# Kernel tuning notes

Hardware: AMD Instinct MI355X
Metric: run time of the kernel (lower is better)

The kernel has to match this reference:

```python
import jax, jax.numpy as jnp
import numpy as np

SIGMA = 1.2
SIGMA_SQ = jnp.float32(SIGMA * SIGMA)


def setup_inputs() -> dict:
    key = jax.random.key(0)
    k1, k2, k3 = jax.random.split(key, 3)
    X = jax.random.normal(k1, (32768, 2), dtype=jnp.float32)
    pattern_layer = jax.random.normal(k2, (8192, 2), dtype=jnp.float32)
    W2 = jax.random.normal(k3, (8192,), dtype=jnp.float32)
    return {"X": X, "pattern_layer": pattern_layer, "W2": W2}


def reference(X, pattern_layer, W2):
    # Pairwise squared distances via |a|^2 + |b|^2 - 2 a.b  -> [N, P]
    x_sq = jnp.sum(X * X, axis=1, keepdims=True)              # [N, 1]
    p_sq = jnp.sum(pattern_layer * pattern_layer, axis=1)     # [P]
    cross = X @ pattern_layer.T                               # [N, P]
    Dsq = x_sq + p_sq[None, :] - 2.0 * cross                  # [N, P]
    K = jnp.exp(-Dsq / (2.0 * SIGMA_SQ))                      # RBF kernel [N, P]
    num = K @ W2                                              # [N]
    den = jnp.sum(K, axis=1)                                  # [N]
    return num / den
```

## Files before the change

### kernel.cpp

```cpp
#include <hip/hip_runtime.h>

#define N 32768
#define P 8192
#define MX 8
#define XG 4
#define PH 2
#define THREADS (XG * PH * 64)
#define XPB (XG * MX)
#define NBLK (N / XPB)
#define PAIRS (P / 2)
#define PAIRS_PER_PH (PAIRS / PH)
#define ITERS (PAIRS_PER_PH / 64)

#define RBF_F 0.50093577808645257f

typedef float v2f __attribute__((ext_vector_type(2)));

static __device__ __forceinline__ float fast_exp2(float x) {
#if __has_builtin(__builtin_amdgcn_exp2f)
    return __builtin_amdgcn_exp2f(x);
#else
    return exp2f(x);
#endif
}

__global__ void prep_kernel(const float* __restrict__ pat,
                            const float* __restrict__ w2,
                            float4* __restrict__ c) {
    int q = blockIdx.x * blockDim.x + threadIdx.x;
    if (q < P / 2) {
        float p00 = pat[4 * q + 0], p01 = pat[4 * q + 1];
        float p10 = pat[4 * q + 2], p11 = pat[4 * q + 3];
        float4 a, b;
        a.x = 2.0f * RBF_F * p00;  a.y = 2.0f * RBF_F * p10;
        a.z = 2.0f * RBF_F * p01;  a.w = 2.0f * RBF_F * p11;
        b.x = -RBF_F * (p00 * p00 + p01 * p01);
        b.y = -RBF_F * (p10 * p10 + p11 * p11);
        b.z = w2[2 * q];           b.w = w2[2 * q + 1];
        c[2 * q]     = a;
        c[2 * q + 1] = b;
    }
}

__global__ __launch_bounds__(THREADS, 4) void
rbf_kernel(const float* __restrict__ X,
           const float4* __restrict__ c,
           float* __restrict__ out) {
    const int t    = threadIdx.x;
    const int lane = t & 63;
    const int w    = __builtin_amdgcn_readfirstlane(t >> 6);
    const int xg   = w >> 1;
    const int ph   = w & 1;

    const int xb = blockIdx.x * XPB + xg * MX;
    const float2* Xp = (const float2*)X;
    v2f xs0[MX], xs1[MX];
#pragma unroll
    for (int i = 0; i < MX; ++i) {
        float2 xv = Xp[xb + i];
        xs0[i] = (v2f){xv.x, xv.x};
        xs1[i] = (v2f){xv.y, xv.y};
    }

    v2f num2[MX], den2[MX];
#pragma unroll
    for (int i = 0; i < MX; ++i) {
        num2[i] = (v2f){0.f, 0.f};
        den2[i] = (v2f){0.f, 0.f};
    }

    const float4* __restrict__ C4w =
        c + (size_t)ph * (2 * PAIRS_PER_PH) + 2 * lane;

#pragma unroll
    for (int j = 0; j < ITERS; ++j) {
        float4 a = C4w[(j << 7)];
        float4 b = C4w[(j << 7) + 1];
#pragma unroll
        for (int i = 0; i < MX; ++i) {
            v2f tt = __builtin_elementwise_fma((v2f){a.x, a.y}, xs0[i],
                                               (v2f){b.x, b.y});
            tt = __builtin_elementwise_fma((v2f){a.z, a.w}, xs1[i], tt);
            v2f k = (v2f){fast_exp2(tt.x), fast_exp2(tt.y)};
            den2[i] += k;
            num2[i] = __builtin_elementwise_fma(k, (v2f){b.z, b.w}, num2[i]);
        }
    }

    float num[MX], den[MX];
#pragma unroll
    for (int i = 0; i < MX; ++i) {
        num[i] = num2[i].x + num2[i].y;
        den[i] = den2[i].x + den2[i].y;
    }
#pragma unroll
    for (int m = 1; m < 64; m <<= 1) {
#pragma unroll
        for (int i = 0; i < MX; ++i) {
            num[i] += __shfl_xor(num[i], m, 64);
            den[i] += __shfl_xor(den[i], m, 64);
        }
    }

    __shared__ float red[XG][PH][MX][2];
    if (lane == 0) {
#pragma unroll
        for (int i = 0; i < MX; ++i) {
            red[xg][ph][i][0] = num[i];
            red[xg][ph][i][1] = den[i];
        }
    }
    __syncthreads();

    if (t < XPB) {
        int g = t >> 3, xi = t & 7;
        float nn = red[g][0][xi][0] + red[g][1][xi][0];
        float dd = red[g][0][xi][1] + red[g][1][xi][1];
        out[blockIdx.x * XPB + t] = nn / dd;
    }
}

extern "C" void kernel_launch(void* const* d_in, const int* in_sizes, int n_in,
                              void* d_out, int out_size, void* d_ws, size_t ws_size,
                              hipStream_t stream) {
    const float* X   = (const float*)d_in[0];
    const float* pat = (const float*)d_in[1];
    const float* w2  = (const float*)d_in[2];
    float* out = (float*)d_out;
    float4* c = (float4*)d_ws;

    prep_kernel<<<(P / 2 + 255) / 256, 256, 0, stream>>>(pat, w2, c);
    rbf_kernel<<<NBLK, THREADS, 0, stream>>>(X, c, out);
}
```

Baseline: 96.26 us.

## Compute RBF cross terms with bf16 split-precision MFMA and fold norm into weights

Replaces the scalar FMA computation of the exponent with 32x32x16 bf16 MFMA. Each fp32 coordinate is split into hi/lo bf16 parts so the cross products keep near-fp32 accuracy. The pattern-norm term exp2(-|p|^2) is moved into precomputed per-pattern weights for numerator and denominator, so the inner loop holds only the MFMA, exp2 and two FMAs per element. The main risks are accuracy loss from the dropped x-norm factor and the bf16 split, possible underflow of the folded exponent factors, and a permuted layout that depends on the exact MFMA output ordering.

```diff
diff --git a/kernel.cpp b/kernel.cpp
--- a/kernel.cpp
+++ b/kernel.cpp
@@ -2,19 +2,18 @@
 
 #define N 32768
 #define P 8192
-#define MX 8
-#define XG 4
-#define PH 2
-#define THREADS (XG * PH * 64)
-#define XPB (XG * MX)
-#define NBLK (N / XPB)
-#define PAIRS (P / 2)
-#define PAIRS_PER_PH (PAIRS / PH)
-#define ITERS (PAIRS_PER_PH / 64)
+#define NBLK (N / 32)
+#define THREADS 512
+#define SLICES 8
+#define PT (P / 32)
+#define TPW (PT / SLICES)
 
 #define RBF_F 0.50093577808645257f
 
-typedef float v2f __attribute__((ext_vector_type(2)));
+typedef float  v2f    __attribute__((ext_vector_type(2)));
+typedef float  f32x4  __attribute__((ext_vector_type(4)));
+typedef float  f32x16 __attribute__((ext_vector_type(16)));
+typedef short  s16x8  __attribute__((ext_vector_type(8)));
 
 static __device__ __forceinline__ float fast_exp2(float x) {
 #if __has_builtin(__builtin_amdgcn_exp2f)
@@ -24,99 +23,141 @@
 #endif
 }
 
+static __device__ __forceinline__ unsigned short f2bf(float f) {
+    unsigned u = __float_as_uint(f);
+    u += 0x7FFF + ((u >> 16) & 1);
+    return (unsigned short)(u >> 16);
+}
+static __device__ __forceinline__ float bf2f(unsigned short h) {
+    return __uint_as_float((unsigned)h << 16);
+}
+
 __global__ void prep_kernel(const float* __restrict__ pat,
                             const float* __restrict__ w2,
-                            float4* __restrict__ c) {
-    int q = blockIdx.x * blockDim.x + threadIdx.x;
-    if (q < P / 2) {
-        float p00 = pat[4 * q + 0], p01 = pat[4 * q + 1];
-        float p10 = pat[4 * q + 2], p11 = pat[4 * q + 3];
-        float4 a, b;
-        a.x = 2.0f * RBF_F * p00;  a.y = 2.0f * RBF_F * p10;
-        a.z = 2.0f * RBF_F * p01;  a.w = 2.0f * RBF_F * p11;
-        b.x = -RBF_F * (p00 * p00 + p01 * p01);
-        b.y = -RBF_F * (p10 * p10 + p11 * p11);
-        b.z = w2[2 * q];           b.w = w2[2 * q + 1];
-        c[2 * q]     = a;
-        c[2 * q + 1] = b;
-    }
+                            s16x8* __restrict__ afrag,
+                            float* __restrict__ wperm,
+                            float* __restrict__ eperm) {
+    int p = blockIdx.x * blockDim.x + threadIdx.x;
+    if (p >= P) return;
+    float p0 = pat[2 * p], p1 = pat[2 * p + 1];
+    float P0 = 2.0f * RBF_F * p0, P1 = 2.0f * RBF_F * p1;
+    unsigned short h0 = f2bf(P0);
+    unsigned short l0 = f2bf(P0 - bf2f(h0));
+    unsigned short h1 = f2bf(P1);
+    unsigned short l1 = f2bf(P1 - bf2f(h1));
+    unsigned short H0 = f2bf(bf2f(h0) * 0.5f), L0 = f2bf(bf2f(l0) * 0.5f);
+    unsigned short H1 = f2bf(bf2f(h1) * 0.5f), L1 = f2bf(bf2f(l1) * 0.5f);
+    s16x8 a;
+    a[0] = (short)H0; a[1] = (short)H0; a[2] = (short)L0;
+    a[3] = (short)H1; a[4] = (short)H1; a[5] = (short)L1;
+    a[6] = 0;         a[7] = 0;
+    int tile = p >> 5, row = p & 31;
+    afrag[tile * 32 + row] = a;
+
+    float c2 = -RBF_F * (p0 * p0 + p1 * p1);
+    float e  = exp2f(c2);
+    float wp = w2[p] * e;
+    int g = (row >> 2) & 1;
+    int r = (row & 3) | (((row >> 3) & 3) << 2);
+    wperm[(tile * 2 + g) * 16 + r] = wp;
+    eperm[(tile * 2 + g) * 16 + r] = e;
 }
+
+#define MFMA(A, B, C) __builtin_amdgcn_mfma_f32_32x32x16_bf16((A), (B), (C), 0, 0, 0)
+
+#define ACC4(D, Wq, Eq, base)                                                 \
+    den2 = __builtin_elementwise_fma((v2f){(D)[base], (D)[base + 1]},         \
+             (v2f){(Eq)[0], (Eq)[1]}, den2);                                  \
+    num2 = __builtin_elementwise_fma((v2f){(D)[base], (D)[base + 1]},         \
+             (v2f){(Wq)[0], (Wq)[1]}, num2);                                  \
+    den2 = __builtin_elementwise_fma((v2f){(D)[base + 2], (D)[base + 3]},     \
+             (v2f){(Eq)[2], (Eq)[3]}, den2);                                  \
+    num2 = __builtin_elementwise_fma((v2f){(D)[base + 2], (D)[base + 3]},     \
+             (v2f){(Wq)[2], (Wq)[3]}, num2);
 
 __global__ __launch_bounds__(THREADS, 4) void
 rbf_kernel(const float* __restrict__ X,
-           const float4* __restrict__ c,
+           const s16x8* __restrict__ afrag,
+           const f32x4* __restrict__ wperm4,
+           const f32x4* __restrict__ eperm4,
            float* __restrict__ out) {
     const int t    = threadIdx.x;
     const int lane = t & 63;
-    const int w    = __builtin_amdgcn_readfirstlane(t >> 6);
-    const int xg   = w >> 1;
-    const int ph   = w & 1;
+    const int wv   = __builtin_amdgcn_readfirstlane(t >> 6);
+    const int col  = lane & 31;
+    const int g    = lane >> 5;
 
-    const int xb = blockIdx.x * XPB + xg * MX;
-    const float2* Xp = (const float2*)X;
-    v2f xs0[MX], xs1[MX];
+    float2 xv = ((const float2*)X)[blockIdx.x * 32 + col];
+    unsigned short xh0 = f2bf(xv.x), xl0 = f2bf(xv.x - bf2f(xh0));
+    unsigned short xh1 = f2bf(xv.y), xl1 = f2bf(xv.y - bf2f(xh1));
+    s16x8 bx;
+    bx[0] = (short)xh0; bx[1] = (short)xl0; bx[2] = (short)xh0;
+    bx[3] = (short)xh1; bx[4] = (short)xl1; bx[5] = (short)xh1;
+    bx[6] = 0;          bx[7] = 0;
+
+    f32x16 Z;
 #pragma unroll
-    for (int i = 0; i < MX; ++i) {
-        float2 xv = Xp[xb + i];
-        xs0[i] = (v2f){xv.x, xv.x};
-        xs1[i] = (v2f){xv.y, xv.y};
+    for (int i = 0; i < 16; ++i) Z[i] = 0.0f;
+
+    const int tile0 = wv * TPW;
+    const s16x8* __restrict__ Ap = afrag + tile0 * 32 + col;
+    const f32x4* __restrict__ Wp = wperm4 + (tile0 * 2 + g) * 4;
+    const f32x4* __restrict__ Ep = eperm4 + (tile0 * 2 + g) * 4;
+
+    s16x8 Af0 = Ap[0];
+    s16x8 Af1 = Ap[32];
+    f32x16 D0 = MFMA(Af0, bx, Z);
+    f32x16 D1;
+
+    v2f num2 = (v2f){0.f, 0.f}, den2 = (v2f){0.f, 0.f};
+
+    for (int tt = 0; tt < TPW; tt += 2) {
+        D1 = MFMA(Af1, bx, Z);
+        Af0 = Ap[((tt + 2) & (TPW - 1)) * 32];
+        f32x4 Wa0 = Wp[tt * 8 + 0], Wa1 = Wp[tt * 8 + 1];
+        f32x4 Wa2 = Wp[tt * 8 + 2], Wa3 = Wp[tt * 8 + 3];
+        f32x4 Ea0 = Ep[tt * 8 + 0], Ea1 = Ep[tt * 8 + 1];
+        f32x4 Ea2 = Ep[tt * 8 + 2], Ea3 = Ep[tt * 8 + 3];
+#pragma unroll
+        for (int i = 0; i < 16; ++i) D0[i] = fast_exp2(D0[i]);
+        ACC4(D0, Wa0, Ea0, 0)
+        ACC4(D0, Wa1, Ea1, 4)
+        ACC4(D0, Wa2, Ea2, 8)
+        ACC4(D0, Wa3, Ea3, 12)
+        D0 = MFMA(Af0, bx, Z);
+        Af1 = Ap[((tt + 3) & (TPW - 1)) * 32];
+        f32x4 Wb0 = Wp[(tt + 1) * 8 + 0], Wb1 = Wp[(tt + 1) * 8 + 1];
+        f32x4 Wb2 = Wp[(tt + 1) * 8 + 2], Wb3 = Wp[(tt + 1) * 8 + 3];
+        f32x4 Eb0 = Ep[(tt + 1) * 8 + 0], Eb1 = Ep[(tt + 1) * 8 + 1];
+        f32x4 Eb2 = Ep[(tt + 1) * 8 + 2], Eb3 = Ep[(tt + 1) * 8 + 3];
+#pragma unroll
+        for (int i = 0; i < 16; ++i) D1[i] = fast_exp2(D1[i]);
+        ACC4(D1, Wb0, Eb0, 0)
+        ACC4(D1, Wb1, Eb1, 4)
+        ACC4(D1, Wb2, Eb2, 8)
+        ACC4(D1, Wb3, Eb3, 12)
     }
 
-    v2f num2[MX], den2[MX];
-#pragma unroll
-    for (int i = 0; i < MX; ++i) {
-        num2[i] = (v2f){0.f, 0.f};
-        den2[i] = (v2f){0.f, 0.f};
-    }
+    float num = num2.x + num2.y;
+    float den = den2.x + den2.y;
+    num += __shfl_xor(num, 32, 64);
+    den += __shfl_xor(den, 32, 64);
 
-    const float4* __restrict__ C4w =
-        c + (size_t)ph * (2 * PAIRS_PER_PH) + 2 * lane;
-
-#pragma unroll
-    for (int j = 0; j < ITERS; ++j) {
-        float4 a = C4w[(j << 7)];
-        float4 b = C4w[(j << 7) + 1];
-#pragma unroll
-        for (int i = 0; i < MX; ++i) {
-            v2f tt = __builtin_elementwise_fma((v2f){a.x, a.y}, xs0[i],
-                                               (v2f){b.x, b.y});
-            tt = __builtin_elementwise_fma((v2f){a.z, a.w}, xs1[i], tt);
-            v2f k = (v2f){fast_exp2(tt.x), fast_exp2(tt.y)};
-            den2[i] += k;
-            num2[i] = __builtin_elementwise_fma(k, (v2f){b.z, b.w}, num2[i]);
-        }
-    }
-
-    float num[MX], den[MX];
-#pragma unroll
-    for (int i = 0; i < MX; ++i) {
-        num[i] = num2[i].x + num2[i].y;
-        den[i] = den2[i].x + den2[i].y;
-    }
-#pragma unroll
-    for (int m = 1; m < 64; m <<= 1) {
-#pragma unroll
-        for (int i = 0; i < MX; ++i) {
-            num[i] += __shfl_xor(num[i], m, 64);
-            den[i] += __shfl_xor(den[i], m, 64);
-        }
-    }
-
-    __shared__ float red[XG][PH][MX][2];
-    if (lane == 0) {
-#pragma unroll
-        for (int i = 0; i < MX; ++i) {
-            red[xg][ph][i][0] = num[i];
-            red[xg][ph][i][1] = den[i];
-        }
+    __shared__ float red[SLICES][32][2];
+    if (lane < 32) {
+        red[wv][lane][0] = num;
+        red[wv][lane][1] = den;
     }
     __syncthreads();
 
-    if (t < XPB) {
-        int g = t >> 3, xi = t & 7;
-        float nn = red[g][0][xi][0] + red[g][1][xi][0];
-        float dd = red[g][0][xi][1] + red[g][1][xi][1];
-        out[blockIdx.x * XPB + t] = nn / dd;
+    if (t < 32) {
+        float nn = 0.f, dd = 0.f;
+#pragma unroll
+        for (int s = 0; s < SLICES; ++s) {
+            nn += red[s][t][0];
+            dd += red[s][t][1];
+        }
+        out[blockIdx.x * 32 + t] = nn / dd;
     }
 }
 
@@ -127,8 +168,14 @@
     const float* pat = (const float*)d_in[1];
     const float* w2  = (const float*)d_in[2];
     float* out = (float*)d_out;
-    float4* c = (float4*)d_ws;
 
-    prep_kernel<<<(P / 2 + 255) / 256, 256, 0, stream>>>(pat, w2, c);
-    rbf_kernel<<<NBLK, THREADS, 0, stream>>>(X, c, out);
+    char* ws = (char*)d_ws;
+    s16x8* afrag = (s16x8*)ws;
+    float* wperm = (float*)(ws + (size_t)P * 16);
+    float* eperm = (float*)(ws + (size_t)P * 16 + (size_t)PT * 2 * 16 * 4);
+
+    prep_kernel<<<(P + 255) / 256, 256, 0, stream>>>(pat, w2, afrag, wperm, eperm);
+    rbf_kernel<<<NBLK, THREADS, 0, stream>>>(X, afrag,
+                                             (const f32x4*)wperm,
+                                             (const f32x4*)eperm, out);
 }
```

Result: slower. 123.2 us (+28.0%).
